# Kernel tuning notes

Hardware: AMD Instinct MI355X
Metric: run time of the kernel (lower is better)

Reference implementation:

```python
import jax, jax.numpy as jnp
import numpy as np

N = 50000   # nodes (and num_graphs, since batch = arange(N))
E = 800000  # edges
F_IN, F_HID, F_OUT = 512, 256, 60


def _gcn_conv(x, src, dst, W, b, n):
    """PyG GCNConv: x' = D^{-1/2} (A+I) D^{-1/2} (x W) + b."""
    h = x @ W                                    # [n, f_out]
    loops = jnp.arange(n)
    s = jnp.concatenate([src, loops])            # add self loops
    d = jnp.concatenate([dst, loops])
    deg = jax.ops.segment_sum(jnp.ones_like(s, dtype=h.dtype), d, num_segments=n)
    dis = jnp.where(deg > 0, jax.lax.rsqrt(jnp.maximum(deg, 1.0)), 0.0)
    norm = dis[s] * dis[d]                       # [E+n]
    msg = h[s] * norm[:, None]                   # gather + per-edge scale
    return jax.ops.segment_sum(msg, d, num_segments=n) + b


def setup_inputs() -> dict:
    key = jax.random.key(0)
    ks = jax.random.split(key, 8)
    x = jax.random.normal(ks[0], (N, F_IN), dtype=jnp.float32)
    edge_index = jax.random.randint(ks[1], (2, E), 0, N)
    batch = jnp.arange(N)  # each node its own graph (see notes: conv3 runs after pooling)
    W1 = jax.random.normal(ks[2], (F_IN, F_HID), dtype=jnp.float32) / np.float32(np.sqrt(F_IN))
    b1 = jnp.zeros((F_HID,), dtype=jnp.float32)
    W2 = jax.random.normal(ks[3], (F_HID, F_HID), dtype=jnp.float32) / np.float32(np.sqrt(F_HID))
    b2 = jnp.zeros((F_HID,), dtype=jnp.float32)
    W3 = jax.random.normal(ks[4], (F_HID, F_OUT), dtype=jnp.float32) / np.float32(np.sqrt(F_HID))
    b3 = jnp.zeros((F_OUT,), dtype=jnp.float32)
    return {"x": x, "edge_index": edge_index, "batch": batch,
            "W1": W1, "b1": b1, "W2": W2, "b2": b2, "W3": W3, "b3": b3}


def reference(x, edge_index, batch, W1, b1, W2, b2, W3, b3):
    src, dst = edge_index[0], edge_index[1]
    n = x.shape[0]
    h = jax.nn.relu(_gcn_conv(x, src, dst, W1, b1, n))
    h = jax.nn.relu(_gcn_conv(h, src, dst, W2, b2, n))
    # global_mean_pool over `batch` (num_graphs == N here since batch = arange)
    cnt = jax.ops.segment_sum(jnp.ones((n,), h.dtype), batch, num_segments=N)
    tot = jax.ops.segment_sum(h, batch, num_segments=N)
    p = tot / jnp.maximum(cnt, 1.0)[:, None]
    # dropout p=0.5 is identity in eval mode
    return _gcn_conv(p, src, dst, W3, b3, N)
```

## Files before the change

### kernel.cpp

```cpp
#include <hip/hip_runtime.h>

#define N_NODES 50000
#define N_EDGES 800000
#define F_IN    512
#define F_HID   256
#define F_OUT   60
#define SCAN_BLOCKS ((N_NODES + 255) / 256)

typedef __bf16    bf16x8 __attribute__((ext_vector_type(8)));
typedef __bf16    bf16x4 __attribute__((ext_vector_type(4)));
typedef float     f32x4  __attribute__((ext_vector_type(4)));
typedef _Float16  f16x4  __attribute__((ext_vector_type(4)));
typedef _Float16  f16x2  __attribute__((ext_vector_type(2)));

__device__ __forceinline__ int SWZ(int row, int slot) {
    return row * 32 + (((slot) ^ ((row >> 1) & 3)) << 3);
}

__global__ void k_cnt_zero(int* __restrict__ cnt) {
    int i = blockIdx.x * blockDim.x + threadIdx.x;
    if (i < N_NODES) cnt[i] = 0;
}
__global__ void k_deg_count(const int* __restrict__ dst, int* __restrict__ cnt) {
    int i = blockIdx.x * blockDim.x + threadIdx.x;
    if (i < N_EDGES) atomicAdd(&cnt[dst[i]], 1);
}
__global__ void k_dis(const int* __restrict__ cnt, float* __restrict__ dis) {
    int i = blockIdx.x * blockDim.x + threadIdx.x;
    if (i < N_NODES) dis[i] = rsqrtf((float)(cnt[i] + 1));
}
__global__ void k_scan1(const int* __restrict__ cnt, int* __restrict__ scanned,
                        int* __restrict__ blocksum) {
    __shared__ int tmp[256];
    int i = blockIdx.x * 256 + threadIdx.x;
    int v = (i < N_NODES) ? cnt[i] : 0;
    tmp[threadIdx.x] = v;
    __syncthreads();
    for (int off = 1; off < 256; off <<= 1) {
        int t = (threadIdx.x >= off) ? tmp[threadIdx.x - off] : 0;
        __syncthreads();
        tmp[threadIdx.x] += t;
        __syncthreads();
    }
    if (i < N_NODES) scanned[i] = tmp[threadIdx.x] - v;
    if (threadIdx.x == 255) blocksum[blockIdx.x] = tmp[255];
}
__global__ void k_scan2(const int* __restrict__ blocksum, int* __restrict__ blockoff) {
    __shared__ int tmp[256];
    int v = (threadIdx.x < SCAN_BLOCKS) ? blocksum[threadIdx.x] : 0;
    tmp[threadIdx.x] = v;
    __syncthreads();
    for (int off = 1; off < 256; off <<= 1) {
        int t = (threadIdx.x >= off) ? tmp[threadIdx.x - off] : 0;
        __syncthreads();
        tmp[threadIdx.x] += t;
        __syncthreads();
    }
    if (threadIdx.x < SCAN_BLOCKS) blockoff[threadIdx.x] = tmp[threadIdx.x] - v;
}
__global__ void k_scan3(const int* __restrict__ scanned, const int* __restrict__ blockoff,
                        int* __restrict__ row_ptr, int* __restrict__ cursor) {
    int i = blockIdx.x * 256 + threadIdx.x;
    if (i < N_NODES) {
        int rp = scanned[i] + blockoff[blockIdx.x];
        row_ptr[i] = rp;
        cursor[i] = rp;
    }
    if (i == 0) row_ptr[N_NODES] = N_EDGES;
}
__global__ void k_fill(const int* __restrict__ src, const int* __restrict__ dst,
                       int* __restrict__ cursor, int* __restrict__ esrc) {
    int e = blockIdx.x * blockDim.x + threadIdx.x;
    if (e < N_EDGES) {
        int pos = atomicAdd(&cursor[dst[e]], 1);
        esrc[pos] = src[e];
    }
}

__global__ void k_cvt_wT(const float* __restrict__ W, __bf16* __restrict__ th,
                         __bf16* __restrict__ tl, int K, int N, int NP) {
    int i = blockIdx.x * 256 + threadIdx.x;
    if (i >= NP * K) return;
    int n = i / K, k = i - n * K;
    float w = (n < N) ? W[(size_t)k * N + n] : 0.f;
    __bf16 h = (__bf16)w;
    th[i] = h;
    tl[i] = (__bf16)(w - (float)h);
}

template<bool A_FP32>
__global__ __launch_bounds__(256)
void k_gemm_n256(const float* __restrict__ Af,
                 const __bf16* __restrict__ Ahi, const __bf16* __restrict__ Alo,
                 const __bf16* __restrict__ Bth, const __bf16* __restrict__ Btl,
                 _Float16* __restrict__ H, int M, int K)
{
    __shared__ __bf16 smem[20480];
    __bf16* sAh = smem;
    __bf16* sAl = smem + 2048;
    __bf16* sBh = smem + 4096;
    __bf16* sBl = smem + 12288;

    const int tid = threadIdx.x;
    const int m0 = blockIdx.y * 64;
    const int lane = tid & 63;
    const int wn = tid >> 6;

    f32x4 acc[4][4];
#pragma unroll
    for (int f = 0; f < 4; ++f)
#pragma unroll
        for (int g = 0; g < 4; ++g)
            acc[f][g] = (f32x4){0.f, 0.f, 0.f, 0.f};

    for (int k0 = 0; k0 < K; k0 += 32) {
        {
            int row = tid >> 2, slot = tid & 3;
            int gm = m0 + row;
            if (A_FP32) {
                float av[8];
                if (gm < M) {
                    const float* p = Af + (size_t)gm * K + k0 + slot * 8;
                    *(float4*)&av[0] = *(const float4*)(p);
                    *(float4*)&av[4] = *(const float4*)(p + 4);
                } else {
#pragma unroll
                    for (int j = 0; j < 8; ++j) av[j] = 0.f;
                }
                bf16x8 h, l;
#pragma unroll
                for (int j = 0; j < 8; ++j) {
                    __bf16 hh = (__bf16)av[j];
                    h[j] = hh; l[j] = (__bf16)(av[j] - (float)hh);
                }
                *(bf16x8*)&sAh[SWZ(row, slot)] = h;
                *(bf16x8*)&sAl[SWZ(row, slot)] = l;
            } else {
                bf16x8 vh = {}, vl = {};
                if (gm < M) {
                    vh = *(const bf16x8*)(Ahi + (size_t)gm * K + k0 + slot * 8);
                    vl = *(const bf16x8*)(Alo + (size_t)gm * K + k0 + slot * 8);
                }
                *(bf16x8*)&sAh[SWZ(row, slot)] = vh;
                *(bf16x8*)&sAl[SWZ(row, slot)] = vl;
            }
        }
#pragma unroll
        for (int it = 0; it < 4; ++it) {
            int c = tid + it * 256;
            int row = c >> 2, slot = c & 3;
            size_t off = (size_t)row * K + k0 + slot * 8;
            *(bf16x8*)&sBh[SWZ(row, slot)] = *(const bf16x8*)(Bth + off);
            *(bf16x8*)&sBl[SWZ(row, slot)] = *(const bf16x8*)(Btl + off);
        }
        __syncthreads();

        bf16x8 ah[4], al[4], bh[4], bl[4];
#pragma unroll
        for (int f = 0; f < 4; ++f) {
            int r = f * 16 + (lane & 15);
            ah[f] = *(const bf16x8*)&sAh[SWZ(r, lane >> 4)];
            al[f] = *(const bf16x8*)&sAl[SWZ(r, lane >> 4)];
        }
#pragma unroll
        for (int g = 0; g < 4; ++g) {
            int r = wn * 64 + g * 16 + (lane & 15);
            bh[g] = *(const bf16x8*)&sBh[SWZ(r, lane >> 4)];
            bl[g] = *(const bf16x8*)&sBl[SWZ(r, lane >> 4)];
        }
#pragma unroll
        for (int f = 0; f < 4; ++f)
#pragma unroll
            for (int g = 0; g < 4; ++g) {
                acc[f][g] = __builtin_amdgcn_mfma_f32_16x16x32_bf16(ah[f], bh[g], acc[f][g], 0, 0, 0);
                acc[f][g] = __builtin_amdgcn_mfma_f32_16x16x32_bf16(al[f], bh[g], acc[f][g], 0, 0, 0);
                acc[f][g] = __builtin_amdgcn_mfma_f32_16x16x32_bf16(ah[f], bl[g], acc[f][g], 0, 0, 0);
            }
        __syncthreads();
    }

#pragma unroll
    for (int f = 0; f < 4; ++f)
#pragma unroll
        for (int g = 0; g < 4; ++g) {
            int col = wn * 64 + g * 16 + (lane & 15);
#pragma unroll
            for (int r = 0; r < 4; ++r) {
                int row = m0 + f * 16 + (lane >> 4) * 4 + r;
                if (row < M) H[(size_t)row * 256 + col] = (_Float16)acc[f][g][r];
            }
        }
}

__global__ __launch_bounds__(256)
void k_gemm_n64(const __bf16* __restrict__ Ahi, const __bf16* __restrict__ Alo,
                const __bf16* __restrict__ Bth, const __bf16* __restrict__ Btl,
                _Float16* __restrict__ H, int M, int N, int K)
{
    __shared__ __bf16 smem[12288];
    __bf16* sAh = smem;
    __bf16* sAl = smem + 4096;
    __bf16* sBh = smem + 8192;
    __bf16* sBl = smem + 10240;

    const int tid = threadIdx.x;
    const int m0 = blockIdx.y * 128;
    const int lane = tid & 63, wid = tid >> 6;
    const int wm = wid >> 1, wn = wid & 1;

    f32x4 acc[4][2];
#pragma unroll
    for (int f = 0; f < 4; ++f)
#pragma unroll
        for (int g = 0; g < 2; ++g)
            acc[f][g] = (f32x4){0.f, 0.f, 0.f, 0.f};

    for (int k0 = 0; k0 < K; k0 += 32) {
#pragma unroll
        for (int it = 0; it < 2; ++it) {
            int c = tid + it * 256;
            int row = c >> 2, slot = c & 3;
            int gm = m0 + row;
            bf16x8 vh = {}, vl = {};
            if (gm < M) {
                vh = *(const bf16x8*)(Ahi + (size_t)gm * K + k0 + slot * 8);
                vl = *(const bf16x8*)(Alo + (size_t)gm * K + k0 + slot * 8);
            }
            *(bf16x8*)&sAh[SWZ(row, slot)] = vh;
            *(bf16x8*)&sAl[SWZ(row, slot)] = vl;
        }
        {
            int row = tid >> 2, slot = tid & 3;
            size_t off = (size_t)row * K + k0 + slot * 8;
            *(bf16x8*)&sBh[SWZ(row, slot)] = *(const bf16x8*)(Bth + off);
            *(bf16x8*)&sBl[SWZ(row, slot)] = *(const bf16x8*)(Btl + off);
        }
        __syncthreads();

        bf16x8 ah[4], al[4], bh[2], bl[2];
#pragma unroll
        for (int f = 0; f < 4; ++f) {
            int r = wm * 64 + f * 16 + (lane & 15);
            ah[f] = *(const bf16x8*)&sAh[SWZ(r, lane >> 4)];
            al[f] = *(const bf16x8*)&sAl[SWZ(r, lane >> 4)];
        }
#pragma unroll
        for (int g = 0; g < 2; ++g) {
            int r = wn * 32 + g * 16 + (lane & 15);
            bh[g] = *(const bf16x8*)&sBh[SWZ(r, lane >> 4)];
            bl[g] = *(const bf16x8*)&sBl[SWZ(r, lane >> 4)];
        }
#pragma unroll
        for (int f = 0; f < 4; ++f)
#pragma unroll
            for (int g = 0; g < 2; ++g) {
                acc[f][g] = __builtin_amdgcn_mfma_f32_16x16x32_bf16(ah[f], bh[g], acc[f][g], 0, 0, 0);
                acc[f][g] = __builtin_amdgcn_mfma_f32_16x16x32_bf16(al[f], bh[g], acc[f][g], 0, 0, 0);
                acc[f][g] = __builtin_amdgcn_mfma_f32_16x16x32_bf16(ah[f], bl[g], acc[f][g], 0, 0, 0);
            }
        __syncthreads();
    }

#pragma unroll
    for (int f = 0; f < 4; ++f)
#pragma unroll
        for (int g = 0; g < 2; ++g) {
            int col = wn * 32 + g * 16 + (lane & 15);
            if (col >= N) continue;
#pragma unroll
            for (int r = 0; r < 4; ++r) {
                int row = m0 + wm * 64 + f * 16 + (lane >> 4) * 4 + r;
                if (row < M) H[(size_t)row * N + col] = (_Float16)acc[f][g][r];
            }
        }
}

__global__ __launch_bounds__(256)
void k_gather256(const _Float16* __restrict__ H, const int* __restrict__ row_ptr,
                 const int* __restrict__ esrc, const float* __restrict__ dis,
                 const float* __restrict__ bias,
                 __bf16* __restrict__ Ghi, __bf16* __restrict__ Glo)
{
    int wid = threadIdx.x >> 6, lane = threadIdx.x & 63;
    int v = blockIdx.x * 4 + wid;
    if (v >= N_NODES) return;
    const f16x4* H4 = (const f16x4*)H;
    float dv = dis[v], d2 = dv * dv;
    float4 b = ((const float4*)bias)[lane];
    f16x4 hv = H4[(size_t)v * 64 + lane];
    float a0 = fmaf((float)hv[0], d2, b.x);
    float a1 = fmaf((float)hv[1], d2, b.y);
    float a2 = fmaf((float)hv[2], d2, b.z);
    float a3 = fmaf((float)hv[3], d2, b.w);

    int e = row_ptr[v], e1 = row_ptr[v + 1];
    for (; e + 7 < e1; e += 8) {
        int s[8];
        float n[8];
        f16x4 h[8];
#pragma unroll
        for (int j = 0; j < 8; ++j) s[j] = esrc[e + j];
#pragma unroll
        for (int j = 0; j < 8; ++j) n[j] = dis[s[j]] * dv;
#pragma unroll
        for (int j = 0; j < 8; ++j) h[j] = H4[(size_t)s[j] * 64 + lane];
#pragma unroll
        for (int j = 0; j < 8; ++j) {
            a0 = fmaf((float)h[j][0], n[j], a0);
            a1 = fmaf((float)h[j][1], n[j], a1);
            a2 = fmaf((float)h[j][2], n[j], a2);
            a3 = fmaf((float)h[j][3], n[j], a3);
        }
    }
    for (; e < e1; ++e) {
        int s = esrc[e];
        float nn = dis[s] * dv;
        f16x4 h = H4[(size_t)s * 64 + lane];
        a0 = fmaf((float)h[0], nn, a0); a1 = fmaf((float)h[1], nn, a1);
        a2 = fmaf((float)h[2], nn, a2); a3 = fmaf((float)h[3], nn, a3);
    }
    a0 = fmaxf(a0, 0.f); a1 = fmaxf(a1, 0.f);
    a2 = fmaxf(a2, 0.f); a3 = fmaxf(a3, 0.f);

    bf16x4 h, l;
    h[0] = (__bf16)a0; l[0] = (__bf16)(a0 - (float)h[0]);
    h[1] = (__bf16)a1; l[1] = (__bf16)(a1 - (float)h[1]);
    h[2] = (__bf16)a2; l[2] = (__bf16)(a2 - (float)h[2]);
    h[3] = (__bf16)a3; l[3] = (__bf16)(a3 - (float)h[3]);
    size_t o = (size_t)v * 256 + lane * 4;
    *(bf16x4*)&Ghi[o] = h;
    *(bf16x4*)&Glo[o] = l;
}

__global__ __launch_bounds__(256)
void k_gather60(const _Float16* __restrict__ H3, const int* __restrict__ row_ptr,
                const int* __restrict__ esrc, const float* __restrict__ dis,
                const float* __restrict__ b3, float* __restrict__ out)
{
    int wid = threadIdx.x >> 6, lane = threadIdx.x & 63;
    int v = blockIdx.x * 4 + wid;
    if (v >= N_NODES || lane >= 30) return;
    const f16x2* H2 = (const f16x2*)H3;
    float dv = dis[v], d2 = dv * dv;
    f16x2 hv = H2[(size_t)v * 30 + lane];
    float a0 = fmaf((float)hv[0], d2, b3[lane * 2]);
    float a1 = fmaf((float)hv[1], d2, b3[lane * 2 + 1]);
    int e = row_ptr[v], e1 = row_ptr[v + 1];
    for (; e + 1 < e1; e += 2) {
        int s0 = esrc[e], s1 = esrc[e + 1];
        float n0 = dis[s0] * dv, n1 = dis[s1] * dv;
        f16x2 h0 = H2[(size_t)s0 * 30 + lane];
        f16x2 h1 = H2[(size_t)s1 * 30 + lane];
        a0 = fmaf((float)h0[0], n0, a0); a1 = fmaf((float)h0[1], n0, a1);
        a0 = fmaf((float)h1[0], n1, a0); a1 = fmaf((float)h1[1], n1, a1);
    }
    if (e < e1) {
        int s = esrc[e];
        float n = dis[s] * dv;
        f16x2 h = H2[(size_t)s * 30 + lane];
        a0 = fmaf((float)h[0], n, a0); a1 = fmaf((float)h[1], n, a1);
    }
    out[(size_t)v * 60 + lane * 2]     = a0;
    out[(size_t)v * 60 + lane * 2 + 1] = a1;
}

extern "C" void kernel_launch(void* const* d_in, const int* in_sizes, int n_in,
                              void* d_out, int out_size, void* d_ws, size_t ws_size,
                              hipStream_t stream)
{
    const float* x  = (const float*)d_in[0];
    const int*   ei = (const int*)d_in[1];
    const float* W1 = (const float*)d_in[3];
    const float* b1 = (const float*)d_in[4];
    const float* W2 = (const float*)d_in[5];
    const float* b2 = (const float*)d_in[6];
    const float* W3 = (const float*)d_in[7];
    const float* b3 = (const float*)d_in[8];
    float* out = (float*)d_out;

    const int* src = ei;
    const int* dst = ei + N_EDGES;

    char* ws = (char*)d_ws;
    int*      cnt      = (int*)(ws + 0);
    float*    dis      = (float*)(ws + 200704);
    int*      scanned  = (int*)(ws + 401408);
    int*      blocksum = (int*)(ws + 602112);
    int*      blockoff = (int*)(ws + 603136);
    int*      row_ptr  = (int*)(ws + 604160);
    int*      cursor   = (int*)(ws + 805376);
    int*      esrc     = (int*)(ws + 1006080);
    __bf16*   w1h      = (__bf16*)(ws + 4206592);
    __bf16*   w1l      = (__bf16*)(ws + 4468736);
    __bf16*   w2h      = (__bf16*)(ws + 4730880);
    __bf16*   w2l      = (__bf16*)(ws + 4861952);
    __bf16*   w3h      = (__bf16*)(ws + 4993024);
    __bf16*   w3l      = (__bf16*)(ws + 5025792);
    _Float16* H        = (_Float16*)(ws + 5058560);
    __bf16*   Ghi      = (__bf16*)(ws + 30658560);
    __bf16*   Glo      = (__bf16*)(ws + 56258560);
    _Float16* H3       = (_Float16*)(ws + 81858560);

    k_cnt_zero<<<SCAN_BLOCKS, 256, 0, stream>>>(cnt);
    k_deg_count<<<(N_EDGES + 255) / 256, 256, 0, stream>>>(dst, cnt);
    k_dis<<<SCAN_BLOCKS, 256, 0, stream>>>(cnt, dis);
    k_scan1<<<SCAN_BLOCKS, 256, 0, stream>>>(cnt, scanned, blocksum);
    k_scan2<<<1, 256, 0, stream>>>(blocksum, blockoff);
    k_scan3<<<SCAN_BLOCKS, 256, 0, stream>>>(scanned, blockoff, row_ptr, cursor);
    k_fill<<<(N_EDGES + 255) / 256, 256, 0, stream>>>(src, dst, cursor, esrc);

    k_cvt_wT<<<(256 * 512 + 255) / 256, 256, 0, stream>>>(W1, w1h, w1l, 512, 256, 256);
    k_cvt_wT<<<(256 * 256 + 255) / 256, 256, 0, stream>>>(W2, w2h, w2l, 256, 256, 256);
    k_cvt_wT<<<(64 * 256 + 255) / 256, 256, 0, stream>>>(W3, w3h, w3l, 256, 60, 64);

    const int MB64  = (N_NODES + 63) / 64;
    const int MB128 = (N_NODES + 127) / 128;
    const int GB    = (N_NODES + 3) / 4;

    k_gemm_n256<true><<<dim3(1, MB64), 256, 0, stream>>>(x, nullptr, nullptr, w1h, w1l,
                                                         H, N_NODES, F_IN);
    k_gather256<<<GB, 256, 0, stream>>>(H, row_ptr, esrc, dis, b1, Ghi, Glo);
    k_gemm_n256<false><<<dim3(1, MB64), 256, 0, stream>>>(nullptr, Ghi, Glo, w2h, w2l,
                                                          H, N_NODES, F_HID);
    k_gather256<<<GB, 256, 0, stream>>>(H, row_ptr, esrc, dis, b2, Ghi, Glo);
    k_gemm_n64<<<dim3(1, MB128), 256, 0, stream>>>(Ghi, Glo, w3h, w3l, H3, N_NODES, F_OUT, F_HID);
    k_gather60<<<GB, 256, 0, stream>>>(H3, row_ptr, esrc, dis, b3, out);
}
```

Baseline: 527.1 us.

## Enlarge n256 GEMM tile to 128 rows and prefetch next K-tile into registers

The 256-wide GEMM kernel now uses 512 threads (8 waves, 2x4) over a 128-row M tile, which halves how often each block reloads the shared B (weight) tile. Global loads for the next K slice are issued into registers before the MFMA loop runs, so memory latency overlaps compute. The barrier moves to the top of the loop. The cost is higher register pressure per thread and fewer resident blocks because of the larger LDS footprint.

```diff
diff --git a/kernel.cpp b/kernel.cpp
--- a/kernel.cpp
+++ b/kernel.cpp
@@ -89,22 +89,55 @@
 }
 
 template<bool A_FP32>
-__global__ __launch_bounds__(256)
+__global__ __launch_bounds__(512)
 void k_gemm_n256(const float* __restrict__ Af,
                  const __bf16* __restrict__ Ahi, const __bf16* __restrict__ Alo,
                  const __bf16* __restrict__ Bth, const __bf16* __restrict__ Btl,
                  _Float16* __restrict__ H, int M, int K)
 {
-    __shared__ __bf16 smem[20480];
+    __shared__ __bf16 smem[24576];
     __bf16* sAh = smem;
-    __bf16* sAl = smem + 2048;
-    __bf16* sBh = smem + 4096;
-    __bf16* sBl = smem + 12288;
+    __bf16* sAl = smem + 4096;
+    __bf16* sBh = smem + 8192;
+    __bf16* sBl = smem + 16384;
 
     const int tid = threadIdx.x;
-    const int m0 = blockIdx.y * 64;
-    const int lane = tid & 63;
-    const int wn = tid >> 6;
+    const int m0 = blockIdx.y * 128;
+    const int lane = tid & 63, wid = tid >> 6;
+    const int wm = wid >> 2, wn = wid & 3;
+
+    const int arow = tid >> 2, aslot = tid & 3;
+    const int brow = tid >> 1, bslot0 = (tid & 1) * 2;
+    const int gm = m0 + arow;
+
+    float  avf[8];
+    bf16x8 avh = {}, avl = {};
+    bf16x8 bvh0, bvh1, bvl0, bvl1;
+
+    auto load_tile = [&](int k0) {
+        if (A_FP32) {
+            if (gm < M) {
+                const float* p = Af + (size_t)gm * K + k0 + aslot * 8;
+                *(float4*)&avf[0] = *(const float4*)(p);
+                *(float4*)&avf[4] = *(const float4*)(p + 4);
+            } else {
+#pragma unroll
+                for (int j = 0; j < 8; ++j) avf[j] = 0.f;
+            }
+        } else {
+            if (gm < M) {
+                avh = *(const bf16x8*)(Ahi + (size_t)gm * K + k0 + aslot * 8);
+                avl = *(const bf16x8*)(Alo + (size_t)gm * K + k0 + aslot * 8);
+            } else {
+                avh = (bf16x8){}; avl = (bf16x8){};
+            }
+        }
+        size_t off = (size_t)brow * K + k0 + bslot0 * 8;
+        bvh0 = *(const bf16x8*)(Bth + off);
+        bvh1 = *(const bf16x8*)(Bth + off + 8);
+        bvl0 = *(const bf16x8*)(Btl + off);
+        bvl1 = *(const bf16x8*)(Btl + off + 8);
+    };
 
     f32x4 acc[4][4];
 #pragma unroll
@@ -113,52 +146,33 @@
         for (int g = 0; g < 4; ++g)
             acc[f][g] = (f32x4){0.f, 0.f, 0.f, 0.f};
 
+    load_tile(0);
+
     for (int k0 = 0; k0 < K; k0 += 32) {
-        {
-            int row = tid >> 2, slot = tid & 3;
-            int gm = m0 + row;
-            if (A_FP32) {
-                float av[8];
-                if (gm < M) {
-                    const float* p = Af + (size_t)gm * K + k0 + slot * 8;
-                    *(float4*)&av[0] = *(const float4*)(p);
-                    *(float4*)&av[4] = *(const float4*)(p + 4);
-                } else {
-#pragma unroll
-                    for (int j = 0; j < 8; ++j) av[j] = 0.f;
-                }
-                bf16x8 h, l;
-#pragma unroll
-                for (int j = 0; j < 8; ++j) {
-                    __bf16 hh = (__bf16)av[j];
-                    h[j] = hh; l[j] = (__bf16)(av[j] - (float)hh);
-                }
-                *(bf16x8*)&sAh[SWZ(row, slot)] = h;
-                *(bf16x8*)&sAl[SWZ(row, slot)] = l;
-            } else {
-                bf16x8 vh = {}, vl = {};
-                if (gm < M) {
-                    vh = *(const bf16x8*)(Ahi + (size_t)gm * K + k0 + slot * 8);
-                    vl = *(const bf16x8*)(Alo + (size_t)gm * K + k0 + slot * 8);
-                }
-                *(bf16x8*)&sAh[SWZ(row, slot)] = vh;
-                *(bf16x8*)&sAl[SWZ(row, slot)] = vl;
-            }
-        }
-#pragma unroll
-        for (int it = 0; it < 4; ++it) {
-            int c = tid + it * 256;
-            int row = c >> 2, slot = c & 3;
-            size_t off = (size_t)row * K + k0 + slot * 8;
-            *(bf16x8*)&sBh[SWZ(row, slot)] = *(const bf16x8*)(Bth + off);
-            *(bf16x8*)&sBl[SWZ(row, slot)] = *(const bf16x8*)(Btl + off);
-        }
+        if (k0) __syncthreads();
+        if (A_FP32) {
+            bf16x8 h, l;
+#pragma unroll
+            for (int j = 0; j < 8; ++j) {
+                __bf16 hh = (__bf16)avf[j];
+                h[j] = hh; l[j] = (__bf16)(avf[j] - (float)hh);
+            }
+            *(bf16x8*)&sAh[SWZ(arow, aslot)] = h;
+            *(bf16x8*)&sAl[SWZ(arow, aslot)] = l;
+        } else {
+            *(bf16x8*)&sAh[SWZ(arow, aslot)] = avh;
+            *(bf16x8*)&sAl[SWZ(arow, aslot)] = avl;
+        }
+        *(bf16x8*)&sBh[SWZ(brow, bslot0)]     = bvh0;
+        *(bf16x8*)&sBh[SWZ(brow, bslot0 + 1)] = bvh1;
+        *(bf16x8*)&sBl[SWZ(brow, bslot0)]     = bvl0;
+        *(bf16x8*)&sBl[SWZ(brow, bslot0 + 1)] = bvl1;
         __syncthreads();
 
         bf16x8 ah[4], al[4], bh[4], bl[4];
 #pragma unroll
         for (int f = 0; f < 4; ++f) {
-            int r = f * 16 + (lane & 15);
+            int r = wm * 64 + f * 16 + (lane & 15);
             ah[f] = *(const bf16x8*)&sAh[SWZ(r, lane >> 4)];
             al[f] = *(const bf16x8*)&sAl[SWZ(r, lane >> 4)];
         }
@@ -168,6 +182,9 @@
             bh[g] = *(const bf16x8*)&sBh[SWZ(r, lane >> 4)];
             bl[g] = *(const bf16x8*)&sBl[SWZ(r, lane >> 4)];
         }
+
+        if (k0 + 32 < K) load_tile(k0 + 32);
+
 #pragma unroll
         for (int f = 0; f < 4; ++f)
 #pragma unroll
@@ -176,7 +193,6 @@
                 acc[f][g] = __builtin_amdgcn_mfma_f32_16x16x32_bf16(al[f], bh[g], acc[f][g], 0, 0, 0);
                 acc[f][g] = __builtin_amdgcn_mfma_f32_16x16x32_bf16(ah[f], bl[g], acc[f][g], 0, 0, 0);
             }
-        __syncthreads();
     }
 
 #pragma unroll
@@ -186,7 +202,7 @@
             int col = wn * 64 + g * 16 + (lane & 15);
 #pragma unroll
             for (int r = 0; r < 4; ++r) {
-                int row = m0 + f * 16 + (lane >> 4) * 4 + r;
+                int row = m0 + wm * 64 + f * 16 + (lane >> 4) * 4 + r;
                 if (row < M) H[(size_t)row * 256 + col] = (_Float16)acc[f][g][r];
             }
         }
@@ -413,15 +429,14 @@
     k_cvt_wT<<<(256 * 256 + 255) / 256, 256, 0, stream>>>(W2, w2h, w2l, 256, 256, 256);
     k_cvt_wT<<<(64 * 256 + 255) / 256, 256, 0, stream>>>(W3, w3h, w3l, 256, 60, 64);
 
-    const int MB64  = (N_NODES + 63) / 64;
     const int MB128 = (N_NODES + 127) / 128;
     const int GB    = (N_NODES + 3) / 4;
 
-    k_gemm_n256<true><<<dim3(1, MB64), 256, 0, stream>>>(x, nullptr, nullptr, w1h, w1l,
-                                                         H, N_NODES, F_IN);
+    k_gemm_n256<true><<<dim3(1, MB128), 512, 0, stream>>>(x, nullptr, nullptr, w1h, w1l,
+                                                          H, N_NODES, F_IN);
     k_gather256<<<GB, 256, 0, stream>>>(H, row_ptr, esrc, dis, b1, Ghi, Glo);
-    k_gemm_n256<false><<<dim3(1, MB64), 256, 0, stream>>>(nullptr, Ghi, Glo, w2h, w2l,
-                                                          H, N_NODES, F_HID);
+    k_gemm_n256<false><<<dim3(1, MB128), 512, 0, stream>>>(nullptr, Ghi, Glo, w2h, w2l,
+                                                           H, N_NODES, F_HID);
     k_gather256<<<GB, 256, 0, stream>>>(H, row_ptr, esrc, dis, b2, Ghi, Glo);
     k_gemm_n64<<<dim3(1, MB128), 256, 0, stream>>>(Ghi, Glo, w3h, w3l, H3, N_NODES, F_OUT, F_HID);
     k_gather60<<<GB, 256, 0, stream>>>(H3, row_ptr, esrc, dis, b3, out);
```

New measurement: 524.1 us. No clear change (-0.6%).
